# Performance work log

Measured on AMD Instinct MI355X. Metric: run time of the kernel, lower is better.

Reference implementation:

```python
import jax, jax.numpy as jnp
import numpy as np

B, T, H, M = 64, 1024, 512, 256  # batch, max_time, out_dim(=annot_dim), memory_dim


def setup_inputs() -> dict:
    key = jax.random.key(0)
    ks = jax.random.split(key, 13)
    s = lambda k, shape, scale=1.0: jax.random.normal(k, shape, dtype=jnp.float32) * scale
    return {
        "memory": s(ks[0], (B, M)),
        "context": s(ks[1], (B, H)),
        "rnn_state": s(ks[2], (B, H)),
        "annotations": s(ks[3], (B, T, H)),
        "W_ih": s(ks[4], (3 * H, H + M), 0.04),
        "b_ih": s(ks[5], (3 * H,), 0.04),
        "W_hh": s(ks[6], (3 * H, H), 0.04),
        "b_hh": s(ks[7], (3 * H,), 0.04),
        "Wq": s(ks[8], (H, H), 0.04),
        "bq": s(ks[9], (H,), 0.04),
        "Wa": s(ks[10], (H, H), 0.04),
        "ba": s(ks[11], (H,), 0.04),
        "v": s(ks[12], (H,), 0.04),
    }


def reference(memory, context, rnn_state, annotations,
              W_ih, b_ih, W_hh, b_hh, Wq, bq, Wa, ba, v):
    # --- GRUCell step (torch semantics) ---
    x = jnp.concatenate([memory, context], axis=-1)          # (B, M+H)
    gi = x @ W_ih.T + b_ih                                   # (B, 3H)
    gh = rnn_state @ W_hh.T + b_hh                           # (B, 3H)
    i_r, i_z, i_n = jnp.split(gi, 3, axis=-1)
    h_r, h_z, h_n = jnp.split(gh, 3, axis=-1)
    r = jax.nn.sigmoid(i_r + h_r)
    z = jax.nn.sigmoid(i_z + h_z)
    n = jnp.tanh(i_n + r * h_n)
    h_new = (1.0 - z) * n + z * rnn_state                    # (B, H)

    # --- Bahdanau additive attention ---
    pq = h_new @ Wq.T + bq                                   # (B, H)
    pa = annotations @ Wa.T + ba                             # (B, T, H)
    scores = jnp.tanh(pq[:, None, :] + pa) @ v               # (B, T)
    align = jax.nn.softmax(scores, axis=-1)                  # (B, T)
    ctx = jnp.einsum('bt,btd->bd', align, annotations)       # (B, H)
    return (h_new, ctx, align)
```

## Files before the change

kernel.cpp:

```cpp
#include <hip/hip_runtime.h>
#include <hip/hip_bf16.h>


typedef __attribute__((ext_vector_type(8))) __bf16 bf16x8;
typedef __attribute__((ext_vector_type(8))) unsigned short u16x8;
typedef __attribute__((ext_vector_type(4))) float f32x4;

__device__ __forceinline__ unsigned short f2bf(float f) {
    __hip_bfloat16 h = __float2bfloat16(f);
    return __builtin_bit_cast(unsigned short, h);
}
__device__ __forceinline__ float tanh_fast(float x) {
    float e = __expf(2.0f * x);
    return 1.0f - 2.0f / (e + 1.0f);
}
__device__ __forceinline__ float sigmoid_f(float x) {
    return 1.0f / (1.0f + __expf(-x));
}
__device__ __forceinline__ int swz(int x) { return x ^ (((x >> 8) & 7) << 4); }

__global__ __launch_bounds__(256) void wconv_kernel(
    const float* __restrict__ W_ih, const float* __restrict__ W_hh,
    const float* __restrict__ Wq, const float* __restrict__ Wa,
    unsigned short* __restrict__ WihB, unsigned short* __restrict__ WhhB,
    unsigned short* __restrict__ WqB, unsigned short* __restrict__ WaB)
{
    const int cb = blockIdx.x * 4 + (threadIdx.x >> 6);
    const int l = threadIdx.x & 63;
    const float* src;
    unsigned short* dst;
    int K, local, NB, kt;
    if (cb < 2304) {
        src = W_ih; dst = WihB; K = 768; local = cb;
        NB = local / 24; kt = local % 24;
    } else if (cb < 3840) {
        src = W_hh; dst = WhhB; K = 512; local = cb - 2304;
        NB = local >> 4; kt = local & 15;
    } else if (cb < 4352) {
        src = Wq; dst = WqB; K = 512; local = cb - 3840;
        NB = local >> 4; kt = local & 15;
    } else {
        src = Wa; dst = WaB; K = 512; local = cb - 4352;
        NB = local >> 4; kt = local & 15;
    }
    const float* s = src + (size_t)(NB * 16 + (l & 15)) * K + kt * 32 + (l >> 4) * 8;
    float4 f0 = *(const float4*)s;
    float4 f1 = *(const float4*)(s + 4);
    u16x8 p;
    p[0] = f2bf(f0.x); p[1] = f2bf(f0.y); p[2] = f2bf(f0.z); p[3] = f2bf(f0.w);
    p[4] = f2bf(f1.x); p[5] = f2bf(f1.y); p[6] = f2bf(f1.z); p[7] = f2bf(f1.w);
    *(u16x8*)&dst[(size_t)local * 512 + l * 8] = p;
}

#define CVT8(f0, f1, AF)                                                           \
    {                                                                              \
        u16x8 p_;                                                                  \
        p_[0] = f2bf((f0).x); p_[1] = f2bf((f0).y); p_[2] = f2bf((f0).z); p_[3] = f2bf((f0).w); \
        p_[4] = f2bf((f1).x); p_[5] = f2bf((f1).y); p_[6] = f2bf((f1).z); p_[7] = f2bf((f1).w); \
        AF = __builtin_bit_cast(bf16x8, p_);                                       \
    }

__global__ __launch_bounds__(64) void gru_kernel(
    const float* __restrict__ memory, const float* __restrict__ context,
    const float* __restrict__ rnn_state,
    const unsigned short* __restrict__ WihB, const float* __restrict__ b_ih,
    const unsigned short* __restrict__ WhhB, const float* __restrict__ b_hh,
    float* __restrict__ h_new)
{
    const int l = threadIdx.x;
    const int mt = blockIdx.x >> 5;
    const int hb = blockIdx.x & 31;
    const int r = l & 15, g = l >> 4;
    const int row = mt * 16 + r;

    f32x4 a_ir = {0,0,0,0}, a_iz = {0,0,0,0}, a_in = {0,0,0,0};
    f32x4 a_hr = {0,0,0,0}, a_hz = {0,0,0,0}, a_hn = {0,0,0,0};

#pragma unroll
    for (int kt = 0; kt < 8; ++kt) {
        const float* s = memory + (size_t)row * 256 + kt * 32 + g * 8;
        float4 f0 = *(const float4*)s, f1 = *(const float4*)(s + 4);
        bf16x8 af; CVT8(f0, f1, af);
        bf16x8 b0 = __builtin_bit_cast(bf16x8, *(const u16x8*)&WihB[((size_t)(hb) * 24 + kt) * 512 + l * 8]);
        bf16x8 b1 = __builtin_bit_cast(bf16x8, *(const u16x8*)&WihB[((size_t)(32 + hb) * 24 + kt) * 512 + l * 8]);
        bf16x8 b2 = __builtin_bit_cast(bf16x8, *(const u16x8*)&WihB[((size_t)(64 + hb) * 24 + kt) * 512 + l * 8]);
        a_ir = __builtin_amdgcn_mfma_f32_16x16x32_bf16(af, b0, a_ir, 0, 0, 0);
        a_iz = __builtin_amdgcn_mfma_f32_16x16x32_bf16(af, b1, a_iz, 0, 0, 0);
        a_in = __builtin_amdgcn_mfma_f32_16x16x32_bf16(af, b2, a_in, 0, 0, 0);
    }
#pragma unroll
    for (int kt = 8; kt < 24; ++kt) {
        const float* s = context + (size_t)row * 512 + (kt - 8) * 32 + g * 8;
        float4 f0 = *(const float4*)s, f1 = *(const float4*)(s + 4);
        bf16x8 af; CVT8(f0, f1, af);
        bf16x8 b0 = __builtin_bit_cast(bf16x8, *(const u16x8*)&WihB[((size_t)(hb) * 24 + kt) * 512 + l * 8]);
        bf16x8 b1 = __builtin_bit_cast(bf16x8, *(const u16x8*)&WihB[((size_t)(32 + hb) * 24 + kt) * 512 + l * 8]);
        bf16x8 b2 = __builtin_bit_cast(bf16x8, *(const u16x8*)&WihB[((size_t)(64 + hb) * 24 + kt) * 512 + l * 8]);
        a_ir = __builtin_amdgcn_mfma_f32_16x16x32_bf16(af, b0, a_ir, 0, 0, 0);
        a_iz = __builtin_amdgcn_mfma_f32_16x16x32_bf16(af, b1, a_iz, 0, 0, 0);
        a_in = __builtin_amdgcn_mfma_f32_16x16x32_bf16(af, b2, a_in, 0, 0, 0);
    }
#pragma unroll
    for (int kt = 0; kt < 16; ++kt) {
        const float* s = rnn_state + (size_t)row * 512 + kt * 32 + g * 8;
        float4 f0 = *(const float4*)s, f1 = *(const float4*)(s + 4);
        bf16x8 af; CVT8(f0, f1, af);
        bf16x8 b0 = __builtin_bit_cast(bf16x8, *(const u16x8*)&WhhB[((size_t)(hb) * 16 + kt) * 512 + l * 8]);
        bf16x8 b1 = __builtin_bit_cast(bf16x8, *(const u16x8*)&WhhB[((size_t)(32 + hb) * 16 + kt) * 512 + l * 8]);
        bf16x8 b2 = __builtin_bit_cast(bf16x8, *(const u16x8*)&WhhB[((size_t)(64 + hb) * 16 + kt) * 512 + l * 8]);
        a_hr = __builtin_amdgcn_mfma_f32_16x16x32_bf16(af, b0, a_hr, 0, 0, 0);
        a_hz = __builtin_amdgcn_mfma_f32_16x16x32_bf16(af, b1, a_hz, 0, 0, 0);
        a_hn = __builtin_amdgcn_mfma_f32_16x16x32_bf16(af, b2, a_hn, 0, 0, 0);
    }
    const int c = hb * 16 + r;
    const float bir = b_ih[c], biz = b_ih[512 + c], bin = b_ih[1024 + c];
    const float bhr = b_hh[c], bhz = b_hh[512 + c], bhn = b_hh[1024 + c];
#pragma unroll
    for (int r2 = 0; r2 < 4; ++r2) {
        const int m = mt * 16 + g * 4 + r2;
        float rr = sigmoid_f(a_ir[r2] + bir + a_hr[r2] + bhr);
        float zz = sigmoid_f(a_iz[r2] + biz + a_hz[r2] + bhz);
        float nn = tanh_fast(a_in[r2] + bin + rr * (a_hn[r2] + bhn));
        float h0 = rnn_state[(size_t)m * 512 + c];
        h_new[(size_t)m * 512 + c] = (1.f - zz) * nn + zz * h0;
    }
}

__global__ __launch_bounds__(64) void pq_kernel(
    const float* __restrict__ h_new, const unsigned short* __restrict__ WqB,
    const float* __restrict__ bq, const float* __restrict__ ba,
    float* __restrict__ q)
{
    const int l = threadIdx.x;
    const int mt = blockIdx.x >> 5;
    const int hb = blockIdx.x & 31;
    const int r = l & 15, g = l >> 4;
    const int row = mt * 16 + r;
    f32x4 acc = {0,0,0,0};
#pragma unroll
    for (int kt = 0; kt < 16; ++kt) {
        const float* s = h_new + (size_t)row * 512 + kt * 32 + g * 8;
        float4 f0 = *(const float4*)s, f1 = *(const float4*)(s + 4);
        bf16x8 af; CVT8(f0, f1, af);
        bf16x8 b0 = __builtin_bit_cast(bf16x8, *(const u16x8*)&WqB[((size_t)hb * 16 + kt) * 512 + l * 8]);
        acc = __builtin_amdgcn_mfma_f32_16x16x32_bf16(af, b0, acc, 0, 0, 0);
    }
    const int c = hb * 16 + r;
    const float add = bq[c] + ba[c];
#pragma unroll
    for (int r2 = 0; r2 < 4; ++r2)
        q[(size_t)(mt * 16 + g * 4 + r2) * 512 + c] = acc[r2] + add;
}

__global__ __launch_bounds__(512, 1) void scores_kernel(
    const float* __restrict__ ann, const unsigned short* __restrict__ WaB,
    const float* __restrict__ qv, const float* __restrict__ v,
    float* __restrict__ scores)
{
    __shared__ unsigned short As[65536];
    __shared__ float s_sc[128];
    const int tid = threadIdx.x;
    const int l = tid & 63;
    const int w = tid >> 6;
    const int r0 = blockIdx.x * 128;
    const int b = blockIdx.x >> 3;

    if (tid < 128) s_sc[tid] = 0.f;

#pragma unroll
    for (int h = 0; h < 2; ++h) {
        float4 f[8][2];
#pragma unroll
        for (int p = 0; p < 8; ++p) {
            int cidx = tid + (h * 8 + p) * 512;
            const float* s = ann + (size_t)(r0 + (cidx >> 6)) * 512 + (cidx & 63) * 8;
            f[p][0] = *(const float4*)s;
            f[p][1] = *(const float4*)(s + 4);
        }
#pragma unroll
        for (int p = 0; p < 8; ++p) {
            int cidx = tid + (h * 8 + p) * 512;
            int row = cidx >> 6;
            int c8 = cidx & 63;
            int kt = c8 >> 2, g = c8 & 3;
            int rtg = row >> 4, r15 = row & 15;
            u16x8 pk;
            pk[0] = f2bf(f[p][0].x); pk[1] = f2bf(f[p][0].y);
            pk[2] = f2bf(f[p][0].z); pk[3] = f2bf(f[p][0].w);
            pk[4] = f2bf(f[p][1].x); pk[5] = f2bf(f[p][1].y);
            pk[6] = f2bf(f[p][1].z); pk[7] = f2bf(f[p][1].w);
            int logical = (((rtg * 16 + kt) * 64) + g * 16 + r15) * 16;
            *(u16x8*)((char*)As + swz(logical)) = pk;
        }
    }

    float qq[4], vv[4];
#pragma unroll
    for (int ct = 0; ct < 4; ++ct) {
        int col = w * 64 + ct * 16 + (l & 15);
        qq[ct] = qv[b * 512 + col];
        vv[ct] = v[col];
    }
    __syncthreads();

    f32x4 acc[8][4];
#pragma unroll
    for (int i = 0; i < 8; ++i)
#pragma unroll
        for (int j = 0; j < 4; ++j) acc[i][j] = (f32x4){0.f, 0.f, 0.f, 0.f};

#define LOADB(BV, ktv)                                                                 \
    {                                                                                  \
        _Pragma("unroll")                                                              \
        for (int ct_ = 0; ct_ < 4; ++ct_)                                              \
            BV[ct_] = *(const u16x8*)(WaB +                                            \
                ((size_t)((w * 4 + ct_) * 16 + (ktv))) * 512 + l * 8);                 \
    }

#define MFMA_K(ktv, BV)                                                                \
    {                                                                                  \
        _Pragma("unroll")                                                              \
        for (int rt_ = 0; rt_ < 8; ++rt_) {                                            \
            int logical = ((rt_ * 16 + (ktv)) * 64 + l) * 16;                          \
            bf16x8 af_ = __builtin_bit_cast(bf16x8,                                    \
                *(const u16x8*)((char*)As + swz(logical)));                            \
            _Pragma("unroll")                                                          \
            for (int ct_ = 0; ct_ < 4; ++ct_)                                          \
                acc[rt_][ct_] = __builtin_amdgcn_mfma_f32_16x16x32_bf16(               \
                    af_, __builtin_bit_cast(bf16x8, BV[ct_]), acc[rt_][ct_], 0, 0, 0); \
        }                                                                              \
    }

    u16x8 bvE[4], bvO[4];
    LOADB(bvE, 0);
    for (int kt2 = 0; kt2 < 8; ++kt2) {
        LOADB(bvO, 2 * kt2 + 1);
        MFMA_K(2 * kt2, bvE);
        if (kt2 < 7) LOADB(bvE, 2 * kt2 + 2);
        MFMA_K(2 * kt2 + 1, bvO);
    }
#undef LOADB
#undef MFMA_K

    float rsum[8][4];
#pragma unroll
    for (int i = 0; i < 8; ++i)
#pragma unroll
        for (int j = 0; j < 4; ++j) rsum[i][j] = 0.f;

#pragma unroll
    for (int ct = 0; ct < 4; ++ct) {
#pragma unroll
        for (int rt = 0; rt < 8; ++rt) {
            f32x4 a = acc[rt][ct];
#pragma unroll
            for (int r2 = 0; r2 < 4; ++r2)
                rsum[rt][r2] += tanh_fast(a[r2] + qq[ct]) * vv[ct];
        }
    }
#pragma unroll
    for (int m = 1; m < 16; m <<= 1) {
#pragma unroll
        for (int rt = 0; rt < 8; ++rt)
#pragma unroll
            for (int r2 = 0; r2 < 4; ++r2)
                rsum[rt][r2] += __shfl_xor(rsum[rt][r2], m, 64);
    }
    if ((l & 15) == 0) {
        int g = l >> 4;
#pragma unroll
        for (int rt = 0; rt < 8; ++rt)
#pragma unroll
            for (int r2 = 0; r2 < 4; ++r2)
                atomicAdd(&s_sc[rt * 16 + g * 4 + r2], rsum[rt][r2]);
    }
    __syncthreads();
    if (tid < 128) scores[r0 + tid] = s_sc[tid];
}

__global__ __launch_bounds__(256) void softmax_kernel(
    const float* __restrict__ scores, float* __restrict__ align_)
{
    const int b = blockIdx.x, tid = threadIdx.x;
    __shared__ float red[256];
    float s[4];
#pragma unroll
    for (int j = 0; j < 4; ++j) s[j] = scores[b * 1024 + j * 256 + tid];
    float mx = fmaxf(fmaxf(s[0], s[1]), fmaxf(s[2], s[3]));
    red[tid] = mx; __syncthreads();
    for (int off = 128; off > 0; off >>= 1) {
        if (tid < off) red[tid] = fmaxf(red[tid], red[tid + off]);
        __syncthreads();
    }
    mx = red[0]; __syncthreads();
    float e[4], sum = 0.f;
#pragma unroll
    for (int j = 0; j < 4; ++j) { e[j] = __expf(s[j] - mx); sum += e[j]; }
    red[tid] = sum; __syncthreads();
    for (int off = 128; off > 0; off >>= 1) {
        if (tid < off) red[tid] += red[tid + off];
        __syncthreads();
    }
    float inv = 1.0f / red[0];
#pragma unroll
    for (int j = 0; j < 4; ++j) align_[b * 1024 + j * 256 + tid] = e[j] * inv;
}

__global__ __launch_bounds__(256) void ctx_part_kernel(
    const float* __restrict__ ann, const float* __restrict__ align_,
    float* __restrict__ part)
{
    const int tid = threadIdx.x;
    const int b = blockIdx.x;
    const int tc = blockIdx.y;
    __shared__ float al[128];
    __shared__ float4 red[128];
    if (tid < 128) al[tid] = align_[b * 1024 + tc * 128 + tid];
    __syncthreads();
    const int rp = tid >> 7, d4 = (tid & 127) * 4;
    const float* ap = ann + ((size_t)(b * 1024 + tc * 128)) * 512 + d4;
    float4 acc = {0.f, 0.f, 0.f, 0.f};
    for (int tt = rp; tt < 128; tt += 2) {
        float4 x = *(const float4*)(ap + (size_t)tt * 512);
        float wv = al[tt];
        acc.x += wv * x.x; acc.y += wv * x.y; acc.z += wv * x.z; acc.w += wv * x.w;
    }
    if (rp == 1) red[tid & 127] = acc;
    __syncthreads();
    if (rp == 0) {
        float4 o = red[tid];
        o.x += acc.x; o.y += acc.y; o.z += acc.z; o.w += acc.w;
        *(float4*)&part[((size_t)(tc * 64 + b)) * 512 + d4] = o;
    }
}

__global__ __launch_bounds__(256) void ctx_reduce_kernel(
    const float* __restrict__ part, float* __restrict__ ctx)
{
    int i4 = (blockIdx.x * 256 + threadIdx.x) * 4;
    float4 s = {0.f, 0.f, 0.f, 0.f};
#pragma unroll
    for (int p = 0; p < 8; ++p) {
        float4 x = *(const float4*)&part[(size_t)p * 32768 + i4];
        s.x += x.x; s.y += x.y; s.z += x.z; s.w += x.w;
    }
    *(float4*)&ctx[i4] = s;
}

extern "C" void kernel_launch(void* const* d_in, const int* in_sizes, int n_in,
                              void* d_out, int out_size, void* d_ws, size_t ws_size,
                              hipStream_t stream)
{
    (void)in_sizes; (void)n_in; (void)out_size; (void)ws_size;
    const float* memory    = (const float*)d_in[0];
    const float* context   = (const float*)d_in[1];
    const float* rnn_state = (const float*)d_in[2];
    const float* ann       = (const float*)d_in[3];
    const float* W_ih      = (const float*)d_in[4];
    const float* b_ih      = (const float*)d_in[5];
    const float* W_hh      = (const float*)d_in[6];
    const float* b_hh      = (const float*)d_in[7];
    const float* Wq        = (const float*)d_in[8];
    const float* bq        = (const float*)d_in[9];
    const float* Wa        = (const float*)d_in[10];
    const float* ba        = (const float*)d_in[11];
    const float* v         = (const float*)d_in[12];

    float* out    = (float*)d_out;
    float* h_new  = out;
    float* ctx    = out + 32768;
    float* align_ = out + 65536;

    char* wsb = (char*)d_ws;
    float* q    = (float*)(wsb + 0);
    float* sc   = (float*)(wsb + 131072);
    float* part = (float*)(wsb + 393216);
    unsigned short* WihB = (unsigned short*)(wsb + 1441792);
    unsigned short* WhhB = (unsigned short*)(wsb + 3801088);
    unsigned short* WqB  = (unsigned short*)(wsb + 5373952);
    unsigned short* WaB  = (unsigned short*)(wsb + 5898240);

    wconv_kernel<<<dim3(1216), dim3(256), 0, stream>>>(
        W_ih, W_hh, Wq, Wa, WihB, WhhB, WqB, WaB);
    gru_kernel<<<dim3(128), dim3(64), 0, stream>>>(
        memory, context, rnn_state, WihB, b_ih, WhhB, b_hh, h_new);
    pq_kernel<<<dim3(128), dim3(64), 0, stream>>>(h_new, WqB, bq, ba, q);
    scores_kernel<<<dim3(512), dim3(512), 0, stream>>>(ann, WaB, q, v, sc);
    softmax_kernel<<<dim3(64), dim3(256), 0, stream>>>(sc, align_);
    ctx_part_kernel<<<dim3(64, 8), dim3(256), 0, stream>>>(ann, align_, part);
    ctx_reduce_kernel<<<dim3(32), dim3(256), 0, stream>>>(part, ctx);
}
```

Measured before the change: 114.5 us.

## Double-buffer scores GEMM with async global-to-LDS loads of fp32 annotations and Wa

Replaces the up-front load-convert-store of the full 128x512 annotation tile into LDS with a K-loop that double-buffers fp32 annotation slices and bf16 Wa slices in LDS via global_load_lds. The bf16 conversion of A moves into the compute loop. LDS drops from 128KB to about 96KB and launch bounds allow 2 blocks per CU. The aim is to overlap global loads with MFMA work and raise occupancy. The cost is a sync every K step, per-tile conversion work, and more register pressure from the 2-block launch bound.

```diff
diff --git a/kernel.cpp b/kernel.cpp
--- a/kernel.cpp
+++ b/kernel.cpp
@@ -17,7 +17,11 @@
 __device__ __forceinline__ float sigmoid_f(float x) {
     return 1.0f / (1.0f + __expf(-x));
 }
-__device__ __forceinline__ int swz(int x) { return x ^ (((x >> 8) & 7) << 4); }
+
+#define GLOAD_LDS16(GSRC, LDST)                                                        \
+    __builtin_amdgcn_global_load_lds(                                                  \
+        (const __attribute__((address_space(1))) unsigned int*)(GSRC),                 \
+        (__attribute__((address_space(3))) unsigned int*)(LDST), 16, 0, 0)
 
 __global__ __launch_bounds__(256) void wconv_kernel(
     const float* __restrict__ W_ih, const float* __restrict__ W_hh,
@@ -152,56 +156,48 @@
         q[(size_t)(mt * 16 + g * 4 + r2) * 512 + c] = acc[r2] + add;
 }
 
-__global__ __launch_bounds__(512, 1) void scores_kernel(
+__global__ __launch_bounds__(512, 2) void scores_kernel(
     const float* __restrict__ ann, const unsigned short* __restrict__ WaB,
     const float* __restrict__ qv, const float* __restrict__ v,
     float* __restrict__ scores)
 {
-    __shared__ unsigned short As[65536];
+    __shared__ __align__(16) char As0[16384];
+    __shared__ __align__(16) char As1[16384];
+    __shared__ __align__(16) char Bs0[32768];
+    __shared__ __align__(16) char Bs1[32768];
     __shared__ float s_sc[128];
+
     const int tid = threadIdx.x;
     const int l = tid & 63;
-    const int w = tid >> 6;
+    const int wv = tid >> 6;
+    const int lq = l & 15;
+    const int g2 = (l >> 4) * 2;
     const int r0 = blockIdx.x * 128;
     const int b = blockIdx.x >> 3;
 
     if (tid < 128) s_sc[tid] = 0.f;
 
-#pragma unroll
-    for (int h = 0; h < 2; ++h) {
-        float4 f[8][2];
-#pragma unroll
-        for (int p = 0; p < 8; ++p) {
-            int cidx = tid + (h * 8 + p) * 512;
-            const float* s = ann + (size_t)(r0 + (cidx >> 6)) * 512 + (cidx & 63) * 8;
-            f[p][0] = *(const float4*)s;
-            f[p][1] = *(const float4*)(s + 4);
-        }
-#pragma unroll
-        for (int p = 0; p < 8; ++p) {
-            int cidx = tid + (h * 8 + p) * 512;
-            int row = cidx >> 6;
-            int c8 = cidx & 63;
-            int kt = c8 >> 2, g = c8 & 3;
-            int rtg = row >> 4, r15 = row & 15;
-            u16x8 pk;
-            pk[0] = f2bf(f[p][0].x); pk[1] = f2bf(f[p][0].y);
-            pk[2] = f2bf(f[p][0].z); pk[3] = f2bf(f[p][0].w);
-            pk[4] = f2bf(f[p][1].x); pk[5] = f2bf(f[p][1].y);
-            pk[6] = f2bf(f[p][1].z); pk[7] = f2bf(f[p][1].w);
-            int logical = (((rtg * 16 + kt) * 64) + g * 16 + r15) * 16;
-            *(u16x8*)((char*)As + swz(logical)) = pk;
-        }
-    }
-
-    float qq[4], vv[4];
-#pragma unroll
-    for (int ct = 0; ct < 4; ++ct) {
-        int col = w * 64 + ct * 16 + (l & 15);
-        qq[ct] = qv[b * 512 + col];
-        vv[ct] = v[col];
-    }
-    __syncthreads();
+    const int sA0 = tid, sA1 = tid + 512;
+    const int rowA0 = sA0 >> 3, rowA1 = sA1 >> 3;
+    const float* asrc0 = ann + (size_t)(r0 + rowA0) * 512 + (((sA0 & 7) ^ (rowA0 & 7)) << 2);
+    const float* asrc1 = ann + (size_t)(r0 + rowA1) * 512 + (((sA1 & 7) ^ (rowA1 & 7)) << 2);
+    const unsigned short* bsrc = WaB + (size_t)(wv * 16) * 512 + l * 8;
+
+#define STAGE(KT, AP, BP)                                                              \
+    {                                                                                  \
+        GLOAD_LDS16(asrc0 + (KT) * 32, (AP) + sA0 * 16);                               \
+        GLOAD_LDS16(asrc1 + (KT) * 32, (AP) + sA1 * 16);                               \
+        _Pragma("unroll")                                                              \
+        for (int j_ = 0; j_ < 4; ++j_) {                                               \
+            GLOAD_LDS16(bsrc + ((size_t)j_ * 8 * 16 + (KT)) * 512,                     \
+                        (BP) + ((wv + j_ * 8) * 64 + l) * 16);                         \
+        }                                                                              \
+    }
+
+    const int swl = lq & 7;
+    const int aoff1 = lq * 128 + (((g2) ^ swl) << 4);
+    const int aoff2 = lq * 128 + (((g2 + 1) ^ swl) << 4);
+    const int boff = ((wv * 4) * 64 + l) * 16;
 
     f32x4 acc[8][4];
 #pragma unroll
@@ -209,38 +205,42 @@
 #pragma unroll
         for (int j = 0; j < 4; ++j) acc[i][j] = (f32x4){0.f, 0.f, 0.f, 0.f};
 
-#define LOADB(BV, ktv)                                                                 \
+#define COMPUTE(AP, BP)                                                                \
     {                                                                                  \
+        u16x8 bv_[4];                                                                  \
         _Pragma("unroll")                                                              \
         for (int ct_ = 0; ct_ < 4; ++ct_)                                              \
-            BV[ct_] = *(const u16x8*)(WaB +                                            \
-                ((size_t)((w * 4 + ct_) * 16 + (ktv))) * 512 + l * 8);                 \
-    }
-
-#define MFMA_K(ktv, BV)                                                                \
-    {                                                                                  \
+            bv_[ct_] = *(const u16x8*)((BP) + boff + ct_ * 1024);                      \
         _Pragma("unroll")                                                              \
-        for (int rt_ = 0; rt_ < 8; ++rt_) {                                            \
-            int logical = ((rt_ * 16 + (ktv)) * 64 + l) * 16;                          \
-            bf16x8 af_ = __builtin_bit_cast(bf16x8,                                    \
-                *(const u16x8*)((char*)As + swz(logical)));                            \
+        for (int mt_ = 0; mt_ < 8; ++mt_) {                                            \
+            f32x4 a1_ = *(const f32x4*)((AP) + aoff1 + mt_ * 2048);                    \
+            f32x4 a2_ = *(const f32x4*)((AP) + aoff2 + mt_ * 2048);                    \
+            u16x8 p_;                                                                  \
+            p_[0] = f2bf(a1_[0]); p_[1] = f2bf(a1_[1]);                                \
+            p_[2] = f2bf(a1_[2]); p_[3] = f2bf(a1_[3]);                                \
+            p_[4] = f2bf(a2_[0]); p_[5] = f2bf(a2_[1]);                                \
+            p_[6] = f2bf(a2_[2]); p_[7] = f2bf(a2_[3]);                                \
+            bf16x8 af_ = __builtin_bit_cast(bf16x8, p_);                               \
             _Pragma("unroll")                                                          \
             for (int ct_ = 0; ct_ < 4; ++ct_)                                          \
-                acc[rt_][ct_] = __builtin_amdgcn_mfma_f32_16x16x32_bf16(               \
-                    af_, __builtin_bit_cast(bf16x8, BV[ct_]), acc[rt_][ct_], 0, 0, 0); \
+                acc[mt_][ct_] = __builtin_amdgcn_mfma_f32_16x16x32_bf16(               \
+                    af_, __builtin_bit_cast(bf16x8, bv_[ct_]), acc[mt_][ct_], 0, 0, 0);\
         }                                                                              \
     }
 
-    u16x8 bvE[4], bvO[4];
-    LOADB(bvE, 0);
-    for (int kt2 = 0; kt2 < 8; ++kt2) {
-        LOADB(bvO, 2 * kt2 + 1);
-        MFMA_K(2 * kt2, bvE);
-        if (kt2 < 7) LOADB(bvE, 2 * kt2 + 2);
-        MFMA_K(2 * kt2 + 1, bvO);
-    }
-#undef LOADB
-#undef MFMA_K
+    STAGE(0, As0, Bs0);
+    __syncthreads();
+#pragma unroll
+    for (int k2 = 0; k2 < 8; ++k2) {
+        STAGE(2 * k2 + 1, As1, Bs1);
+        COMPUTE(As0, Bs0);
+        __syncthreads();
+        if (k2 < 7) STAGE(2 * k2 + 2, As0, Bs0);
+        COMPUTE(As1, Bs1);
+        __syncthreads();
+    }
+#undef STAGE
+#undef COMPUTE
 
     float rsum[8][4];
 #pragma unroll
@@ -250,29 +250,32 @@
 
 #pragma unroll
     for (int ct = 0; ct < 4; ++ct) {
-#pragma unroll
-        for (int rt = 0; rt < 8; ++rt) {
-            f32x4 a = acc[rt][ct];
+        int col = wv * 64 + ct * 16 + lq;
+        float qq = qv[b * 512 + col];
+        float vvv = v[col];
+#pragma unroll
+        for (int mt = 0; mt < 8; ++mt) {
+            f32x4 a = acc[mt][ct];
 #pragma unroll
             for (int r2 = 0; r2 < 4; ++r2)
-                rsum[rt][r2] += tanh_fast(a[r2] + qq[ct]) * vv[ct];
+                rsum[mt][r2] += tanh_fast(a[r2] + qq) * vvv;
         }
     }
 #pragma unroll
     for (int m = 1; m < 16; m <<= 1) {
 #pragma unroll
-        for (int rt = 0; rt < 8; ++rt)
+        for (int mt = 0; mt < 8; ++mt)
 #pragma unroll
             for (int r2 = 0; r2 < 4; ++r2)
-                rsum[rt][r2] += __shfl_xor(rsum[rt][r2], m, 64);
-    }
-    if ((l & 15) == 0) {
+                rsum[mt][r2] += __shfl_xor(rsum[mt][r2], m, 64);
+    }
+    if (lq == 0) {
         int g = l >> 4;
 #pragma unroll
-        for (int rt = 0; rt < 8; ++rt)
+        for (int mt = 0; mt < 8; ++mt)
 #pragma unroll
             for (int r2 = 0; r2 < 4; ++r2)
-                atomicAdd(&s_sc[rt * 16 + g * 4 + r2], rsum[rt][r2]);
+                atomicAdd(&s_sc[mt * 16 + g * 4 + r2], rsum[mt][r2]);
     }
     __syncthreads();
     if (tid < 128) scores[r0 + tid] = s_sc[tid];
```

Result: slower. 119.2 us (+4.2%).
